# Performance work log

Hardware: AMD Instinct MI355X
Metric: run time of the kernel (lower is better)

The kernel has to match this reference:

```python
import jax, jax.numpy as jnp
import numpy as np

B, T, C = 2, 2048, 1024
H = 16
D = C // H          # 64
HID = C // 4        # meta_net bottleneck = 256
FF = 4 * C          # 4096


def setup_inputs() -> dict:
    key = jax.random.key(0)
    ks = jax.random.split(key, 11)
    s = lambda fan_in: 1.0 / np.sqrt(fan_in)
    inp = {
        "x": jax.random.normal(ks[0], (B, T, C), jnp.float32),
        # torch nn.Linear weights are [out, in]
        "Wq": jax.random.uniform(ks[1], (C, C), jnp.float32, -s(C), s(C)),
        "Wk": jax.random.uniform(ks[2], (C, C), jnp.float32, -s(C), s(C)),
        "Wv": jax.random.uniform(ks[3], (C, C), jnp.float32, -s(C), s(C)),
        "Wm1": jax.random.uniform(ks[4], (HID, C), jnp.float32, -s(C), s(C)),
        "bm1": jax.random.uniform(ks[5], (HID,), jnp.float32, -s(C), s(C)),
        "Wm2": jax.random.uniform(ks[6], (H, HID), jnp.float32, -s(HID), s(HID)),
        "bm2": jax.random.uniform(ks[7], (H,), jnp.float32, -s(HID), s(HID)),
        "Wproj": jax.random.uniform(ks[8], (C, C), jnp.float32, -s(C), s(C)),
        "Wfc": jax.random.uniform(ks[9], (FF, C), jnp.float32, -s(C), s(C)),
        "Wcp": jax.random.uniform(ks[10], (C, FF), jnp.float32, -s(FF), s(FF)),
    }
    return inp


def _rms_norm(x):
    eps = jnp.finfo(x.dtype).eps
    return x * jax.lax.rsqrt(jnp.mean(jnp.square(x), axis=-1, keepdims=True) + eps)


def reference(x, Wq, Wk, Wv, Wm1, bm1, Wm2, bm2, Wproj, Wfc, Wcp):
    b, t, c = x.shape
    h = Wm2.shape[0]
    d = c // h
    q = (x @ Wq.T).reshape(b, t, h, d)
    k = (x @ Wk.T).reshape(b, t, h, d)
    v = (x @ Wv.T).reshape(b, t, h, d)
    surprise = jax.nn.sigmoid(jnp.maximum(x @ Wm1.T + bm1, 0.0) @ Wm2.T + bm2)  # [b,t,h]
    decay = 1.0 - surprise

    # time-major for scan: [t, b, h, ...]
    qT = jnp.transpose(q, (1, 0, 2, 3))
    kT = jnp.transpose(k, (1, 0, 2, 3))
    vT = jnp.transpose(v, (1, 0, 2, 3))
    dT = jnp.transpose(decay, (1, 0, 2))     # [t,b,h]
    gT = jnp.transpose(surprise, (1, 0, 2))  # [t,b,h]

    def step(state, inp):
        qt, kt, vt, dt, gt = inp
        # state: [b,h,d,d]; decay-gated rank-1 update
        state = state * dt[..., None, None] + gt[..., None, None] * (kt[..., :, None] * vt[..., None, :])
        yt = jnp.einsum('bhd,bhde->bhe', qt, state)
        return state, yt

    state0 = jnp.zeros((b, h, d, d), x.dtype)
    _, ys = jax.lax.scan(step, state0, (qT, kT, vT, dT, gT))  # ys: [t,b,h,d]
    y = jnp.transpose(ys, (1, 0, 2, 3)).reshape(b, t, c)
    y = y @ Wproj.T
    yn = _rms_norm(y)
    mlp = jnp.square(jnp.maximum(yn @ Wfc.T, 0.0)) @ Wcp.T
    return y + mlp
```

## Files before the change

### kernel.cpp

```cpp
#include <hip/hip_runtime.h>
#include <math.h>

#define BB   2
#define TT   2048
#define CC   1024
#define HH   16
#define DD   64
#define HID  256
#define FFD  4096
#define NTOK (BB*TT)
#define CT   64
#define NC   (TT/CT)
#define NBH  (BB*HH)
#define NCHK (NBH*NC)
#define MB   (1048576ULL)

typedef unsigned short u16;
typedef unsigned int   u32;
typedef __attribute__((ext_vector_type(8))) short frag8;
typedef __attribute__((ext_vector_type(4))) float f32x4;

__device__ __forceinline__ float bf2f(u16 h){
    union { u32 u; float f; } c; c.u = ((u32)h) << 16; return c.f;
}
__device__ __forceinline__ u16 f2bf(float f){
    union { float f; u32 u; } c; c.f = f;
    u32 u = c.u;
    u += 0x7FFFu + ((u >> 16) & 1u);
    return (u16)(u >> 16);
}
__device__ __forceinline__ bool is_f32(const u32* flags, int idx) {
    if (idx == -2) return true;
    if (idx < 0)  return false;
    return flags[idx] != 0;
}

__device__ __forceinline__ void gload16(const void* g, void* l) {
    __builtin_amdgcn_global_load_lds(
        (const __attribute__((address_space(1))) u32*)g,
        (__attribute__((address_space(3))) u32*)l, 16, 0, 0);
}

struct InPtrs { const void* p[11]; int n[11]; };

__global__ __launch_bounds__(64)
void sniff_kernel(InPtrs ip, u32* __restrict__ flags)
{
    int lane = threadIdx.x;
    u32 f0 = 0;
    for (int i = 0; i < 11; i++) {
        const u16* p = (const u16*)ip.p[i];
        int cap = ip.n[i] < 256 ? ip.n[i] : 256;
        bool ok = true;
        for (int j = lane; j < cap; j += 64) {
            u16 u = p[j];
            u32 e = (u >> 7) & 0xFFu;
            bool good = (u == 0u) || (u == 0x8000u) || (e >= 64u && e < 192u);
            ok = ok && good;
        }
        unsigned long long ball = __ballot(ok);
        u32 fl = (ball == ~0ull) ? 0u : 1u;
        if (ip.n[i] < 64) fl = f0;
        if (i == 0) f0 = fl;
        if (lane == 0) flags[i] = fl;
    }
}

struct ConvArgs {
    const void* src[6];
    u16* dst[6];
    int flag[6];
    int bstart[7];
    int nseg;
};

__global__ __launch_bounds__(256)
void conv_kernel(ConvArgs a, const u32* __restrict__ flags)
{
    int b = blockIdx.x;
    int s = 0;
    #pragma unroll
    for (int i = 1; i < 6; i++) if (i < a.nseg && b >= a.bstart[i]) s = i;
    size_t off = ((size_t)(b - a.bstart[s])) * 2048 + (size_t)threadIdx.x * 8;
    u16* d = a.dst[s] + off;
    if (flags[a.flag[s]] != 0) {
        const float* sp = (const float*)a.src[s] + off;
        float4 x0 = *(const float4*)sp;
        float4 x1 = *(const float4*)(sp + 4);
        u16 buf[8];
        buf[0]=f2bf(x0.x); buf[1]=f2bf(x0.y); buf[2]=f2bf(x0.z); buf[3]=f2bf(x0.w);
        buf[4]=f2bf(x1.x); buf[5]=f2bf(x1.y); buf[6]=f2bf(x1.z); buf[7]=f2bf(x1.w);
        *(uint4*)d = *(uint4*)buf;
    } else {
        *(uint4*)d = *(const uint4*)((const u16*)a.src[s] + off);
    }
}

__device__ __forceinline__ void xcd_map(int i, int NB, int gx, int& bm, int& bn)
{
    int per = NB >> 3;
    int iq  = (i & 7) * per + (i >> 3);
    bm = iq / gx;
    bn = iq % gx;
}

template<int MODE, int BM, int BN, int KS>
__global__ __launch_bounds__(256)
void gemm_nt(const u16* __restrict__ A, const u16* __restrict__ B,
             void* Cm, void* Cm2, const void* aux,
             int M, int N, int K, int lda, int ldb,
             const u32* __restrict__ flags, int oi)
{
    constexpr int MFR = BM / 32;
    constexpr int NFR = BN / 32;
    constexpr int BKE = KS * 32;
    const bool of32 = is_f32(flags, oi);
    __shared__ u16 As[2][KS][BM * 32];
    __shared__ u16 Bs[2][KS][BN * 32];
    const int tid = threadIdx.x;
    int bm, bn;
    xcd_map(blockIdx.x, gridDim.x, N / BN, bm, bn);
    const int z = blockIdx.y;
    const size_t koff = (size_t)z * K;

    const int wave = tid >> 6, lane = tid & 63;
    const int lm = lane & 15, quad = lane >> 4;
    const int wm = (wave >> 1) * (BM / 2), wn = (wave & 1) * (BN / 2);

    const int srow = lane >> 2;
    const int scol = (lane & 3) * 8;
    const int arow = (BM == 128) ? (wave*32 + srow) : (wave*16 + srow);
    const int brow = (BN == 128) ? (wave*32 + srow) : (wave*16 + srow);
    const u16* gA = A + (size_t)(bm*BM + arow)*lda + koff + scol;
    const u16* gB = B + (size_t)(bn*BN + brow)*ldb + koff + scol;
    const size_t a16 = (size_t)16 * lda, b16 = (size_t)16 * ldb;

    f32x4 acc[MFR][NFR];
    #pragma unroll
    for (int i = 0; i < MFR; i++)
        #pragma unroll
        for (int j = 0; j < NFR; j++)
            acc[i][j] = (f32x4){0.f, 0.f, 0.f, 0.f};

    auto stage = [&](int buf, int kk) {
        #pragma unroll
        for (int ks = 0; ks < KS; ks++) {
            if constexpr (BM == 128) {
                gload16(gA + kk + ks*32,       &As[buf][ks][wave*1024]);
                gload16(gA + kk + ks*32 + a16, &As[buf][ks][wave*1024 + 512]);
            } else {
                gload16(gA + kk + ks*32, &As[buf][ks][wave*512]);
            }
            if constexpr (BN == 128) {
                gload16(gB + kk + ks*32,       &Bs[buf][ks][wave*1024]);
                gload16(gB + kk + ks*32 + b16, &Bs[buf][ks][wave*1024 + 512]);
            } else {
                gload16(gB + kk + ks*32, &Bs[buf][ks][wave*512]);
            }
        }
    };

    stage(0, 0);
    __syncthreads();
    int cur = 0;
    for (int k0 = 0; k0 < K; k0 += BKE) {
        if (k0 + BKE < K) stage(cur ^ 1, k0 + BKE);
        #pragma unroll
        for (int ks = 0; ks < KS; ks++) {
            frag8 af[MFR], bfr[NFR];
            #pragma unroll
            for (int i = 0; i < MFR; i++)
                af[i]  = *(frag8*)&As[cur][ks][(wm + i*16 + lm)*32 + quad*8];
            #pragma unroll
            for (int j = 0; j < NFR; j++)
                bfr[j] = *(frag8*)&Bs[cur][ks][(wn + j*16 + lm)*32 + quad*8];
            #pragma unroll
            for (int i = 0; i < MFR; i++)
                #pragma unroll
                for (int j = 0; j < NFR; j++)
                    acc[i][j] = __builtin_amdgcn_mfma_f32_16x16x32_bf16(
                        af[i], bfr[j], acc[i][j], 0, 0, 0);
        }
        __syncthreads();
        cur ^= 1;
    }

    float* outF = (float*)(z ? Cm2 : Cm);
    #pragma unroll
    for (int i = 0; i < MFR; i++) {
        #pragma unroll
        for (int j = 0; j < NFR; j++) {
            const int gcol = bn*BN + wn + j*16 + lm;
            #pragma unroll
            for (int r = 0; r < 4; r++) {
                const int grow = bm*BM + wm + i*16 + quad*4 + r;
                size_t off = (size_t)grow * N + gcol;
                float vv = acc[i][j][r];
                if constexpr (MODE == 0) {
                    outF[off] = vv;
                } else if constexpr (MODE == 2) {
                    vv = fmaxf(vv, 0.f);
                    ((u16*)Cm)[off] = f2bf(vv * vv);
                } else {
                    float res = of32 ? ((const float*)aux)[off]
                                     : bf2f(((const u16*)aux)[off]);
                    vv += res;
                    if (of32) ((float*)Cm)[off] = vv;
                    else      ((u16*)Cm)[off]   = f2bf(vv);
                }
            }
        }
    }
}

__global__ __launch_bounds__(256)
void gemm_qkvm(const u16* __restrict__ xb,
               const u16* __restrict__ Wqb, const u16* __restrict__ Wkb,
               const u16* __restrict__ Wvb, const u16* __restrict__ Wm1b,
               const void* __restrict__ bm1,
               u16* __restrict__ q, u16* __restrict__ k, u16* __restrict__ v,
               float* __restrict__ hid, const u32* __restrict__ flags)
{
    __shared__ u16 As[2][128 * 32];
    __shared__ u16 Bs[2][128 * 32];
    const int tid = threadIdx.x;
    int bm, bn;
    xcd_map(blockIdx.x, 832, 26, bm, bn);

    const int bsel = bn >> 3;
    const u16* B = (bsel == 0) ? Wqb : (bsel == 1) ? Wkb
                 : (bsel == 2) ? Wvb : Wm1b;

    const int wave = tid >> 6, lane = tid & 63;
    const int lm = lane & 15, quad = lane >> 4;
    const int wm = (wave >> 1) * 64, wn = (wave & 1) * 64;

    const int srow = lane >> 2;
    const int scol = (lane & 3) * 8;
    const u16* gA = xb + (size_t)(bm*128 + wave*32 + srow)*CC + scol;
    const u16* gB = B + (size_t)((bn & 7)*128 + wave*32 + srow)*CC + scol;
    const size_t s16 = (size_t)16 * CC;

    f32x4 acc[4][4];
    #pragma unroll
    for (int i = 0; i < 4; i++)
        #pragma unroll
        for (int j = 0; j < 4; j++)
            acc[i][j] = (f32x4){0.f, 0.f, 0.f, 0.f};

    auto stage = [&](int buf, int kk) {
        gload16(gA + kk,       &As[buf][wave*1024]);
        gload16(gA + kk + s16, &As[buf][wave*1024 + 512]);
        gload16(gB + kk,       &Bs[buf][wave*1024]);
        gload16(gB + kk + s16, &Bs[buf][wave*1024 + 512]);
    };

    stage(0, 0);
    __syncthreads();
    int cur = 0;
    for (int k0 = 0; k0 < CC; k0 += 32) {
        if (k0 + 32 < CC) stage(cur ^ 1, k0 + 32);
        frag8 af[4], bfr[4];
        #pragma unroll
        for (int i = 0; i < 4; i++) {
            af[i]  = *(frag8*)&As[cur][(wm + i*16 + lm)*32 + quad*8];
            bfr[i] = *(frag8*)&Bs[cur][(wn + i*16 + lm)*32 + quad*8];
        }
        #pragma unroll
        for (int i = 0; i < 4; i++)
            #pragma unroll
            for (int j = 0; j < 4; j++)
                acc[i][j] = __builtin_amdgcn_mfma_f32_16x16x32_bf16(
                    af[i], bfr[j], acc[i][j], 0, 0, 0);
        __syncthreads();
        cur ^= 1;
    }

    if (bsel < 3) {
        u16* outp = (bsel == 0) ? q : (bsel == 1) ? k : v;
        #pragma unroll
        for (int i = 0; i < 4; i++) {
            #pragma unroll
            for (int j = 0; j < 4; j++) {
                const int gcol = (bn & 7)*128 + wn + j*16 + lm;
                #pragma unroll
                for (int r = 0; r < 4; r++) {
                    const int grow = bm*128 + wm + i*16 + quad*4 + r;
                    outp[(size_t)grow * CC + gcol] = f2bf(acc[i][j][r]);
                }
            }
        }
    } else {
        const bool biasf = is_f32(flags, 5);
        #pragma unroll
        for (int i = 0; i < 4; i++) {
            #pragma unroll
            for (int j = 0; j < 4; j++) {
                const int gcol = (bn & 7)*128 + wn + j*16 + lm;
                float bia = biasf ? ((const float*)bm1)[gcol]
                                  : bf2f(((const u16*)bm1)[gcol]);
                #pragma unroll
                for (int r = 0; r < 4; r++) {
                    const int grow = bm*128 + wm + i*16 + quad*4 + r;
                    hid[(size_t)grow * HID + gcol] = fmaxf(acc[i][j][r] + bia, 0.f);
                }
            }
        }
    }
}

__global__ __launch_bounds__(256)
void meta2_kernel(const float* __restrict__ hid, const void* __restrict__ Wm2,
                  const void* __restrict__ bm2, float* __restrict__ g,
                  float* __restrict__ dec, const u32* __restrict__ flags)
{
    const bool wf = is_f32(flags, 6);
    const bool bf = is_f32(flags, 7);
    __shared__ float hs[16][257];
    __shared__ float wsm[16][257];
    int tid  = threadIdx.x;
    int tok0 = blockIdx.x * 16;
    for (int i = tid; i < 16*256; i += 256) {
        wsm[i >> 8][i & 255] = wf ? ((const float*)Wm2)[i] : bf2f(((const u16*)Wm2)[i]);
        hs [i >> 8][i & 255] = hid[(size_t)tok0*256 + i];
    }
    __syncthreads();
    int tok = tid >> 4, hh = tid & 15;
    float s = 0.f;
    #pragma unroll 8
    for (int kk = 0; kk < 256; kk++) s = fmaf(hs[tok][kk], wsm[hh][kk], s);
    s += bf ? ((const float*)bm2)[hh] : bf2f(((const u16*)bm2)[hh]);
    float sg = 1.f / (1.f + expf(-s));
    int idx = (tok0 + tok) * HH + hh;
    g[idx]   = sg;
    dec[idx] = 1.f - sg;
}

__device__ __forceinline__ void cum_prefix(const float* dd, float* cum, int tid)
{
    if (tid < 64) {
        float lw = logf(fmaxf(dd[tid], 1e-30f));
        #pragma unroll
        for (int off = 1; off < 64; off <<= 1) {
            float nv = __shfl_up(lw, off, 64);
            if (tid >= off) lw += nv;
        }
        cum[tid] = lw;
    }
    __syncthreads();
}

__global__ __launch_bounds__(256)
void scan_pass1(const u16* __restrict__ kbuf, const u16* __restrict__ vbuf,
                const float* __restrict__ g, const float* __restrict__ dec,
                float* __restrict__ Mb, float* __restrict__ Pb)
{
    __shared__ u16 kt[64*72];
    __shared__ u16 vt[64*72];
    __shared__ float dd[64], gg[64], cum[64], sw[64];
    int tid = threadIdx.x;
    int bhc = blockIdx.x;
    int c = bhc & 31, h = (bhc >> 5) & 15, b = bhc >> 9;
    int t0 = c * CT;
    size_t rowbase = ((size_t)(b*TT + t0))*CC + h*DD;

    if (tid < 64) {
        int gidx = (b*TT + t0 + tid)*HH + h;
        dd[tid] = dec[gidx];
        gg[tid] = g[gidx];
    }
    __syncthreads();
    cum_prefix(dd, cum, tid);
    float ctot = cum[63];
    if (tid < 64) sw[tid] = gg[tid] * expf(ctot - cum[tid]);
    __syncthreads();

    #pragma unroll 4
    for (int i = tid; i < 4096; i += 256) {
        int ss = i >> 6, d = i & 63;
        size_t gi = rowbase + (size_t)ss*CC + d;
        kt[d*72 + ss] = f2bf(sw[ss] * bf2f(kbuf[gi]));
        vt[d*72 + ss] = vbuf[gi];
    }
    __syncthreads();

    const int w = tid >> 6, lane = tid & 63;
    const int lm = lane & 15, quad = lane >> 4;

    f32x4 mf[4];
    #pragma unroll
    for (int j = 0; j < 4; j++) mf[j] = (f32x4){0.f,0.f,0.f,0.f};
    #pragma unroll
    for (int kk = 0; kk < 2; kk++) {
        frag8 aK = *(frag8*)&kt[(w*16 + lm)*72 + kk*32 + quad*8];
        #pragma unroll
        for (int j = 0; j < 4; j++) {
            frag8 bV = *(frag8*)&vt[(j*16 + lm)*72 + kk*32 + quad*8];
            mf[j] = __builtin_amdgcn_mfma_f32_16x16x32_bf16(aK, bV, mf[j], 0, 0, 0);
        }
    }

    size_t base = (size_t)bhc * 4096;
    #pragma unroll
    for (int r = 0; r < 4; r++) {
        int d = w*16 + quad*4 + r;
        #pragma unroll
        for (int j = 0; j < 4; j++)
            Mb[base + (size_t)d*64 + j*16 + lm] = mf[j][r];
    }
    if (tid == 0) Pb[bhc] = expf(ctot);
}

__global__ __launch_bounds__(256)
void scan_pass2(float* __restrict__ MS, const float* __restrict__ Pb)
{
    int bh = blockIdx.x >> 4, grp = blockIdx.x & 15, tid = threadIdx.x;
    int eo = grp*256 + tid;
    float st = 0.f;
    for (int c = 0; c < NC; c++) {
        size_t e = ((size_t)bh*NC + c) * 4096 + eo;
        float p = Pb[bh*NC + c];
        float m = MS[e];
        MS[e] = st;
        st = fmaf(p, st, m);
    }
}

__global__ __launch_bounds__(256)
void scan_pass3(const u16* __restrict__ qbuf, const u16* __restrict__ kbuf,
                const u16* __restrict__ vbuf, const float* __restrict__ g,
                const float* __restrict__ dec, const float* __restrict__ Sb,
                u16* __restrict__ y)
{
    __shared__ u16 qs16[64*72];
    __shared__ u16 ks16[64*72];
    __shared__ u16 vt16[64*72];
    __shared__ u16 aws16[64*72];
    __shared__ float Ss_t[64*68];
    __shared__ float dd[64], gg[64], cum[64];
    int tid = threadIdx.x;
    int bhc = blockIdx.x;
    int c = bhc & 31, h = (bhc >> 5) & 15, b = bhc >> 9;
    int t0 = c * CT;
    size_t rowbase = ((size_t)(b*TT + t0))*CC + h*DD;
    size_t sbase = (size_t)bhc * 4096;

    {
        int sr = tid >> 2, d0 = (tid & 3) * 16;
        size_t gq = rowbase + (size_t)sr*CC + d0;
        *(uint4*)&qs16[sr*72 + d0]     = *(const uint4*)&qbuf[gq];
        *(uint4*)&qs16[sr*72 + d0 + 8] = *(const uint4*)&qbuf[gq + 8];
        *(uint4*)&ks16[sr*72 + d0]     = *(const uint4*)&kbuf[gq];
        *(uint4*)&ks16[sr*72 + d0 + 8] = *(const uint4*)&kbuf[gq + 8];
        #pragma unroll 4
        for (int i = tid; i < 4096; i += 256) {
            int ss = i >> 6, e = i & 63;
            vt16[e*72 + ss] = vbuf[rowbase + (size_t)ss*CC + e];
        }
        int dr = tid >> 2, e0 = (tid & 3) * 16;
        #pragma unroll
        for (int m = 0; m < 4; m++) {
            float4 sv4 = *(const float4*)&Sb[sbase + (size_t)dr*64 + e0 + m*4];
            Ss_t[(e0 + m*4 + 0)*68 + dr] = sv4.x;
            Ss_t[(e0 + m*4 + 1)*68 + dr] = sv4.y;
            Ss_t[(e0 + m*4 + 2)*68 + dr] = sv4.z;
            Ss_t[(e0 + m*4 + 3)*68 + dr] = sv4.w;
        }
        if (tid < 64) {
            int gidx = (b*TT + t0 + tid)*HH + h;
            dd[tid] = dec[gidx];
            gg[tid] = g[gidx];
        }
    }
    __syncthreads();
    cum_prefix(dd, cum, tid);

    const int w = tid >> 6, lane = tid & 63;
    const int lm = lane & 15, quad = lane >> 4;

    f32x4 a1f[4];
    #pragma unroll
    for (int j = 0; j < 4; j++) a1f[j] = (f32x4){0.f,0.f,0.f,0.f};
    #pragma unroll
    for (int kk = 0; kk < 2; kk++) {
        frag8 aq = *(frag8*)&qs16[(w*16 + lm)*72 + kk*32 + quad*8];
        #pragma unroll
        for (int j = 0; j < 4; j++) {
            frag8 bk = *(frag8*)&ks16[(j*16 + lm)*72 + kk*32 + quad*8];
            a1f[j] = __builtin_amdgcn_mfma_f32_16x16x32_bf16(aq, bk, a1f[j], 0, 0, 0);
        }
    }

    #pragma unroll
    for (int j = 0; j < 4; j++) {
        #pragma unroll
        for (int r = 0; r < 4; r++) {
            int t = w*16 + quad*4 + r, s = j*16 + lm;
            float wgt = (s <= t) ? gg[s] * expf(cum[t] - cum[s]) : 0.f;
            aws16[t*72 + s] = f2bf(wgt * a1f[j][r]);
        }
    }
    __syncthreads();

    f32x4 of[4];
    #pragma unroll
    for (int j = 0; j < 4; j++) of[j] = (f32x4){0.f,0.f,0.f,0.f};
    #pragma unroll
    for (int kk = 0; kk < 2; kk++) {
        frag8 aA = *(frag8*)&aws16[(w*16 + lm)*72 + kk*32 + quad*8];
        #pragma unroll
        for (int j = 0; j < 4; j++) {
            frag8 bV = *(frag8*)&vt16[(j*16 + lm)*72 + kk*32 + quad*8];
            of[j] = __builtin_amdgcn_mfma_f32_16x16x32_bf16(aA, bV, of[j], 0, 0, 0);
        }
    }

    float o2v[4][4] = {};
    for (int d8 = 0; d8 < 8; d8++) {
        frag8 qr[4];
        #pragma unroll
        for (int r = 0; r < 4; r++)
            qr[r] = *(frag8*)&qs16[(w*16 + quad*4 + r)*72 + d8*8];
        float qv[4][8];
        #pragma unroll
        for (int r = 0; r < 4; r++)
            #pragma unroll
            for (int d2 = 0; d2 < 8; d2++)
                qv[r][d2] = bf2f((u16)qr[r][d2]);
        #pragma unroll
        for (int j = 0; j < 4; j++) {
            int e = j*16 + lm;
            float4 s0 = *(float4*)&Ss_t[e*68 + d8*8];
            float4 s1 = *(float4*)&Ss_t[e*68 + d8*8 + 4];
            float sv[8] = {s0.x, s0.y, s0.z, s0.w, s1.x, s1.y, s1.z, s1.w};
            #pragma unroll
            for (int d2 = 0; d2 < 8; d2++)
                #pragma unroll
                for (int r = 0; r < 4; r++)
                    o2v[j][r] = fmaf(qv[r][d2], sv[d2], o2v[j][r]);
        }
    }

    #pragma unroll
    for (int r = 0; r < 4; r++) {
        int t = w*16 + quad*4 + r;
        float cd = expf(cum[t]);
        size_t obase = rowbase + (size_t)t*CC;
        #pragma unroll
        for (int j = 0; j < 4; j++)
            y[obase + j*16 + lm] = f2bf(fmaf(cd, o2v[j][r], of[j][r]));
    }
}

__global__ __launch_bounds__(256)
void rmsnorm_kernel(const float* __restrict__ p0, const float* __restrict__ p1,
                    void* __restrict__ yres, u16* __restrict__ yn,
                    const u32* __restrict__ flags)
{
    const bool of32 = flags[0] != 0;
    __shared__ float red[4];
    __shared__ float sscale;
    int row = blockIdx.x, tid = threadIdx.x;
    size_t base = (size_t)row*CC + tid*4;
    float4 a = *(const float4*)&p0[base];
    float4 b = *(const float4*)&p1[base];
    float v0 = a.x + b.x, v1 = a.y + b.y, v2 = a.z + b.z, v3 = a.w + b.w;
    if (of32) {
        *(float4*)((float*)yres + base) = make_float4(v0, v1, v2, v3);
    } else {
        u16* yr = (u16*)yres + base;
        yr[0] = f2bf(v0); yr[1] = f2bf(v1); yr[2] = f2bf(v2); yr[3] = f2bf(v3);
    }
    float p = v0*v0 + v1*v1 + v2*v2 + v3*v3;
    #pragma unroll
    for (int off = 32; off > 0; off >>= 1) p += __shfl_down(p, off, 64);
    if ((tid & 63) == 0) red[tid >> 6] = p;
    __syncthreads();
    if (tid == 0) {
        float tot = red[0] + red[1] + red[2] + red[3];
        sscale = rsqrtf(tot * (1.0f/1024.0f) + 1.1920928955078125e-07f);
    }
    __syncthreads();
    float sc = sscale;
    yn[base + 0] = f2bf(v0 * sc);
    yn[base + 1] = f2bf(v1 * sc);
    yn[base + 2] = f2bf(v2 * sc);
    yn[base + 3] = f2bf(v3 * sc);
}

extern "C" void kernel_launch(void* const* d_in, const int* in_sizes, int n_in,
                              void* d_out, int out_size, void* d_ws, size_t ws_size,
                              hipStream_t stream)
{
    char* ws = (char*)d_ws;
    u16*   xb     = (u16*)  (ws + 32*MB);
    u16*   Wqb    = (u16*)  (ws + 40*MB);
    u16*   Wkb    = (u16*)  (ws + 42*MB);
    u16*   Wvb    = (u16*)  (ws + 44*MB);
    u16*   Wm1b   = (u16*)  (ws + 46*MB);
    u16*   Wprojb = (u16*)  (ws + 8*MB);
    u16*   q      = (u16*)  (ws + 0*MB);
    u16*   k      = (u16*)  (ws + 16*MB);
    u16*   v      = (u16*)  (ws + 24*MB);
    float* hid    = (float*)(ws + 10*MB);
    float* g      = (float*)(ws + 14*MB);
    float* dec    = (float*)(ws + 14*MB + 262144);
    float* Pb     = (float*)(ws + 14*MB + 524288);
    float* MS     = (float*)(ws + 32*MB);
    u16*   yat    = q;
    float* p0     = (float*)(ws + 16*MB);
    float* p1     = (float*)(ws + 32*MB);
    u16*   yn     = (u16*)  (ws + 0*MB);
    u16*   Wfcb   = (u16*)  (ws + 8*MB);
    u16*   h1     = (u16*)  (ws + 16*MB);
    u16*   Wcpb   = (u16*)  (ws + 0*MB);
    u32*   flags  = (u32*)  (ws + 48*MB);

    InPtrs ip;
    for (int i = 0; i < 11; i++) { ip.p[i] = d_in[i]; ip.n[i] = in_sizes[i]; }
    sniff_kernel<<<1, 64, 0, stream>>>(ip, flags);

    ConvArgs c1{};
    c1.src[0] = d_in[0]; c1.dst[0] = xb;     c1.flag[0] = 0;
    c1.src[1] = d_in[1]; c1.dst[1] = Wqb;    c1.flag[1] = 1;
    c1.src[2] = d_in[2]; c1.dst[2] = Wkb;    c1.flag[2] = 2;
    c1.src[3] = d_in[3]; c1.dst[3] = Wvb;    c1.flag[3] = 3;
    c1.src[4] = d_in[4]; c1.dst[4] = Wm1b;   c1.flag[4] = 4;
    c1.src[5] = d_in[8]; c1.dst[5] = Wprojb; c1.flag[5] = 8;
    {
        int nb[6] = {2048, 512, 512, 512, 128, 512};
        int cum = 0;
        for (int i = 0; i < 6; i++) { c1.bstart[i] = cum; cum += nb[i]; }
        c1.bstart[6] = cum;
        c1.nseg = 6;
        conv_kernel<<<cum, 256, 0, stream>>>(c1, flags);
    }

    gemm_qkvm<<<832, 256, 0, stream>>>(xb, Wqb, Wkb, Wvb, Wm1b, d_in[5],
                                       q, k, v, hid, flags);
    meta2_kernel<<<NTOK/16, 256, 0, stream>>>(hid, d_in[6], d_in[7], g, dec, flags);
    scan_pass1<<<NCHK, 256, 0, stream>>>(k, v, g, dec, MS, Pb);
    scan_pass2<<<NBH*16, 256, 0, stream>>>(MS, Pb);
    scan_pass3<<<NCHK, 256, 0, stream>>>(q, k, v, g, dec, MS, yat);
    gemm_nt<0,128,128,1><<<dim3(256, 2), 256, 0, stream>>>(yat, Wprojb, p0, p1,
        nullptr, NTOK, CC, 512, CC, CC, flags, -2);
    ConvArgs c2{};
    c2.src[0] = d_in[9]; c2.dst[0] = Wfcb; c2.flag[0] = 9;
    c2.bstart[0] = 0; for (int i = 1; i < 7; i++) c2.bstart[i] = 2048;
    c2.nseg = 1;
    conv_kernel<<<2048, 256, 0, stream>>>(c2, flags);
    rmsnorm_kernel<<<NTOK, 256, 0, stream>>>(p0, p1, d_out, yn, flags);
    gemm_nt<2,128,128,1><<<dim3(1024, 1), 256, 0, stream>>>(yn, Wfcb, h1, nullptr,
        nullptr, NTOK, FFD, CC, CC, CC, flags, -1);
    ConvArgs c3{};
    c3.src[0] = d_in[10]; c3.dst[0] = Wcpb; c3.flag[0] = 10;
    c3.bstart[0] = 0; for (int i = 1; i < 7; i++) c3.bstart[i] = 2048;
    c3.nseg = 1;
    conv_kernel<<<2048, 256, 0, stream>>>(c3, flags);
    gemm_nt<3,64,64,2><<<dim3(1024, 1), 256, 0, stream>>>(h1, Wcpb, d_out, nullptr,
        d_out, NTOK, CC, FFD, FFD, FFD, flags, 0);
}
```

Baseline: 380.4 us.

## Add 256x256-tile 8-wave FC GEMM with split-phase prefetch pipeline

Replaces the generic 128x128 gemm_nt for the relu-squared FC projection with a dedicated kernel that uses 256x256 output tiles, 512 threads, a 64-wide K step and double-buffered LDS. Global-to-LDS loads for the next K-tile are issued in four quarter phases, interleaved with MFMA work and guarded by hand-placed vmcnt waits and raw barriers. Larger tiles raise operand reuse and arithmetic intensity per load. The cost is 128KB of LDS per block and only 256 blocks, which limits occupancy, and the hand-written waitcnt and barrier protocol is fragile.

Result: slower. 391.7 us (+3.0%).

```diff
diff --git a/kernel.cpp b/kernel.cpp
--- a/kernel.cpp
+++ b/kernel.cpp
@@ -39,6 +39,15 @@
     __builtin_amdgcn_global_load_lds(
         (const __attribute__((address_space(1))) u32*)g,
         (__attribute__((address_space(3))) u32*)l, 16, 0, 0);
+}
+
+template<int N> __device__ __forceinline__ void wait_vm() {
+    if constexpr (N == 0)      asm volatile("s_waitcnt vmcnt(0)" ::: "memory");
+    else if constexpr (N == 4) asm volatile("s_waitcnt vmcnt(4)" ::: "memory");
+    else                       asm volatile("s_waitcnt vmcnt(6)" ::: "memory");
+}
+__device__ __forceinline__ void barrier_raw() {
+    asm volatile("s_barrier" ::: "memory");
 }
 
 struct InPtrs { const void* p[11]; int n[11]; };
@@ -208,6 +217,109 @@
                     if (of32) ((float*)Cm)[off] = vv;
                     else      ((u16*)Cm)[off]   = f2bf(vv);
                 }
+            }
+        }
+    }
+}
+
+__global__ __launch_bounds__(512)
+void gemm_fc8(const u16* __restrict__ A, const u16* __restrict__ B,
+              u16* __restrict__ C)
+{
+    __shared__ u16 As[2][256 * 64];
+    __shared__ u16 Bs[2][256 * 64];
+    const int tid = threadIdx.x;
+    int bm, bn;
+    xcd_map(blockIdx.x, 256, 16, bm, bn);
+
+    const int w = tid >> 6, lane = tid & 63;
+    const int lm = lane & 15, quad = lane >> 4;
+    const int wm = (w >> 2) * 128, wn = (w & 3) * 64;
+
+    const int srow = tid >> 3;
+    const int scol = (tid & 7) * 8;
+    const u16* gA = A + (size_t)(bm*256 + srow)*1024 + scol;
+    const u16* gB = B + (size_t)(bn*256 + srow)*1024 + scol;
+
+    auto stageA = [&](int buf, int h, int t1) {
+        size_t ko = (size_t)t1 * 64;
+        #pragma unroll
+        for (int q = 0; q < 2; q++)
+            gload16(gA + (size_t)(h*128 + q*64)*1024 + ko,
+                    &As[buf][(h*128 + q*64 + w*8)*64]);
+    };
+    auto stageB = [&](int buf, int h, int t1) {
+        size_t ko = (size_t)t1 * 64;
+        #pragma unroll
+        for (int q = 0; q < 2; q++)
+            gload16(gB + (size_t)(h*128 + q*64)*1024 + ko,
+                    &Bs[buf][(h*128 + q*64 + w*8)*64]);
+    };
+
+    f32x4 acc[8][4];
+    #pragma unroll
+    for (int i = 0; i < 8; i++)
+        #pragma unroll
+        for (int j = 0; j < 4; j++)
+            acc[i][j] = (f32x4){0.f, 0.f, 0.f, 0.f};
+
+    constexpr int NT = 16;
+    stageA(0, 0, 0); stageB(0, 0, 0); stageA(0, 1, 0); stageB(0, 1, 0);
+
+    for (int t = 0; t < NT; ++t) {
+        const int cur = t & 1;
+        const bool more = (t + 1 < NT);
+        #pragma unroll
+        for (int p = 0; p < 4; ++p) {
+            if (more) {
+                if (p == 0)      stageA(cur ^ 1, 0, t + 1);
+                else if (p == 1) stageB(cur ^ 1, 0, t + 1);
+                else if (p == 2) stageA(cur ^ 1, 1, t + 1);
+                else             stageB(cur ^ 1, 1, t + 1);
+            }
+            if (p == 0) { if (more) wait_vm<6>(); else wait_vm<4>(); }
+            if (p == 1) { if (more) wait_vm<4>(); else wait_vm<0>(); }
+            barrier_raw();
+            const int rh = p >> 1, ch = p & 1;
+            frag8 af[4][2], bfr[2][2];
+            #pragma unroll
+            for (int i = 0; i < 4; i++)
+                #pragma unroll
+                for (int kk = 0; kk < 2; kk++)
+                    af[i][kk] = *(frag8*)&As[cur][(wm + rh*64 + i*16 + lm)*64
+                                                  + kk*32 + quad*8];
+            #pragma unroll
+            for (int j = 0; j < 2; j++)
+                #pragma unroll
+                for (int kk = 0; kk < 2; kk++)
+                    bfr[j][kk] = *(frag8*)&Bs[cur][(wn + ch*32 + j*16 + lm)*64
+                                                   + kk*32 + quad*8];
+            __builtin_amdgcn_s_setprio(1);
+            #pragma unroll
+            for (int kk = 0; kk < 2; kk++)
+                #pragma unroll
+                for (int i = 0; i < 4; i++)
+                    #pragma unroll
+                    for (int j = 0; j < 2; j++)
+                        acc[rh*4 + i][ch*2 + j] =
+                            __builtin_amdgcn_mfma_f32_16x16x32_bf16(
+                                af[i][kk], bfr[j][kk], acc[rh*4 + i][ch*2 + j],
+                                0, 0, 0);
+            __builtin_amdgcn_s_setprio(0);
+        }
+    }
+
+    #pragma unroll
+    for (int I = 0; I < 8; I++) {
+        #pragma unroll
+        for (int J = 0; J < 4; J++) {
+            const int gcol = bn*256 + wn + (J >> 1)*32 + (J & 1)*16 + lm;
+            #pragma unroll
+            for (int r = 0; r < 4; r++) {
+                const int grow = bm*256 + wm + (I >> 2)*64 + (I & 3)*16
+                               + quad*4 + r;
+                float vv = fmaxf(acc[I][J][r], 0.f);
+                C[(size_t)grow * FFD + gcol] = f2bf(vv * vv);
             }
         }
     }
@@ -650,8 +762,7 @@
     c2.nseg = 1;
     conv_kernel<<<2048, 256, 0, stream>>>(c2, flags);
     rmsnorm_kernel<<<NTOK, 256, 0, stream>>>(p0, p1, d_out, yn, flags);
-    gemm_nt<2,128,128,1><<<dim3(1024, 1), 256, 0, stream>>>(yn, Wfcb, h1, nullptr,
-        nullptr, NTOK, FFD, CC, CC, CC, flags, -1);
+    gemm_fc8<<<256, 512, 0, stream>>>(yn, Wfcb, h1);
     ConvArgs c3{};
     c3.src[0] = d_in[10]; c3.dst[0] = Wcpb; c3.flag[0] = 10;
     c3.bstart[0] = 0; for (int i = 1; i < 7; i++) c3.bstart[i] = 2048;
```
